# Performance work log

Hardware: AMD Instinct MI355X
Metric: run time of the kernel (lower is better)

Reference implementation:

```python
import jax, jax.numpy as jnp
import numpy as np

N_USER = 50000
N_ITEM = 50000
E = 800000
C_IN = 128
C_OUT = 128
N_HEADS = 4


def setup_inputs() -> dict:
    key = jax.random.key(0)
    ks = jax.random.split(key, 12)
    xav = lambda k, shp: jax.random.uniform(k, shp, jnp.float32, -1.0, 1.0) * jnp.sqrt(6.0 / (shp[0] + shp[1]))
    return {
        'x_user': jax.random.normal(ks[0], (N_USER, C_IN), jnp.float32),
        'x_item': jax.random.normal(ks[1], (N_ITEM, C_IN), jnp.float32),
        'ei_u2i': jnp.stack([jax.random.randint(ks[2], (E,), 0, N_USER, jnp.int32),
                             jax.random.randint(ks[3], (E,), 0, N_ITEM, jnp.int32)]),
        'ei_i2u': jnp.stack([jax.random.randint(ks[4], (E,), 0, N_ITEM, jnp.int32),
                             jax.random.randint(ks[5], (E,), 0, N_USER, jnp.int32)]),
        'W_nb': xav(ks[6], (C_OUT, C_IN)),
        'b_nb': jnp.zeros((C_OUT,), jnp.float32),
        'W_self': xav(ks[7], (C_OUT, C_IN)),
        'b_self': jnp.zeros((C_OUT,), jnp.float32),
        'in_proj_w': xav(ks[8], (3 * C_OUT, C_OUT)),
        'in_proj_b': jnp.zeros((3 * C_OUT,), jnp.float32),
        'out_proj_w': xav(ks[9], (C_OUT, C_OUT)),
        'out_proj_b': jnp.zeros((C_OUT,), jnp.float32),
    }


def _multi_aggr(h_src, edge_index, n_dst):
    """h_src: already lin_neighbor-transformed src features [N_src, C].
    Returns [n_dst, 4, C] stacked as [max, min, sum, mean] (torch_scatter semantics:
    empty segments -> 0; mean divides by clamp(count, 1))."""
    src, dst = edge_index[0], edge_index[1]
    msgs = h_src[src]  # [E, C]  (linear commutes with gather)
    s = jax.ops.segment_sum(msgs, dst, num_segments=n_dst)
    cnt = jax.ops.segment_sum(jnp.ones((msgs.shape[0],), msgs.dtype), dst, num_segments=n_dst)
    has = (cnt > 0)[:, None]
    mean = s / jnp.maximum(cnt, 1.0)[:, None]
    mx = jnp.where(has, jax.ops.segment_max(msgs, dst, num_segments=n_dst), 0.0)
    mn = jnp.where(has, jax.ops.segment_min(msgs, dst, num_segments=n_dst), 0.0)
    return jnp.stack([mx, mn, s, mean], axis=1)  # [n_dst, 4, C]


def _mha(tokens, in_proj_w, in_proj_b, out_proj_w, out_proj_b):
    """torch nn.MultiheadAttention (eval mode, batch_first=False). tokens: [S, N, C]."""
    S, N, C = tokens.shape
    H, Dh = N_HEADS, C // N_HEADS
    qkv = tokens @ in_proj_w.T + in_proj_b            # [S, N, 3C]
    q, k, v = jnp.split(qkv, 3, axis=-1)
    q = q.reshape(S, N, H, Dh) * (1.0 / jnp.sqrt(jnp.asarray(Dh, tokens.dtype)))
    k = k.reshape(S, N, H, Dh)
    v = v.reshape(S, N, H, Dh)
    scores = jnp.einsum('snhd,tnhd->nhst', q, k)       # [N, H, S, S]
    attn = jax.nn.softmax(scores, axis=-1)
    o = jnp.einsum('nhst,tnhd->snhd', attn, v).reshape(S, N, C)
    return o @ out_proj_w.T + out_proj_b               # [S, N, C]


def reference(x_user, x_item, ei_u2i, ei_i2u, W_nb, b_nb, W_self, b_self,
              in_proj_w, in_proj_b, out_proj_w, out_proj_b):
    # shared neighbor linear applied once per node type, then gathered per edge
    h_user = x_user @ W_nb.T + b_nb
    h_item = x_item @ W_nb.T + b_nb
    aggr_item = _multi_aggr(h_user, ei_u2i, N_ITEM)    # user->item : [N_item, 4, C]
    aggr_user = _multi_aggr(h_item, ei_i2u, N_USER)    # item->user : [N_user, 4, C]

    def per_type(x, aggr):
        self_feat = x @ W_self.T + b_self              # [N, C]
        # tokens: [self, max, min, sum, mean] -> [5, N, C]
        tokens = jnp.concatenate([self_feat[None], jnp.transpose(aggr, (1, 0, 2))], axis=0)
        attn_out = _mha(tokens, in_proj_w, in_proj_b, out_proj_w, out_proj_b)
        return self_feat + attn_out.mean(axis=0)

    out_user = per_type(x_user, aggr_user)
    out_item = per_type(x_item, aggr_item)
    return (out_user, out_item)
```

## Files before the change

### kernel.cpp

```cpp
#include <hip/hip_runtime.h>
#include <hip/hip_bf16.h>


#define C 128
#define NHEAD 4
#define DH 32
#define QK_SCALE 0.17677669529663687f

typedef __attribute__((ext_vector_type(8))) short bf16x8;
typedef __attribute__((ext_vector_type(4))) short short4v;
typedef __attribute__((ext_vector_type(2))) short short2v;
typedef __attribute__((ext_vector_type(4))) float f32x4;

__device__ __forceinline__ short f2bf(float f) {
    unsigned u = __float_as_uint(f);
    unsigned r = u + 0x7FFFu + ((u >> 16) & 1u);
    return (short)(r >> 16);
}

__global__ __launch_bounds__(256, 2) void transform_prep_kernel(
    const float* __restrict__ xu, const float* __restrict__ xi,
    int NU, int NTOT,
    const float* __restrict__ Wnb, const float* __restrict__ bnb,
    const float* __restrict__ Wself, const float* __restrict__ bself,
    float* __restrict__ h, float* __restrict__ selfout,
    const float* __restrict__ Wip, unsigned* __restrict__ img,
    int* __restrict__ curA, int nA, int* __restrict__ curB, int nB, int TB)
{
    const int tid = threadIdx.x;

    if ((int)blockIdx.x >= TB) {
        int bid2 = (int)blockIdx.x - TB;
        if (bid2 < 96) {
            int id = bid2 * 256 + tid;
            int ks = id / (384 * 16);
            int rem = id - ks * (384 * 16);
            int n = rem >> 4, kk = rem & 15;
            float a = Wip[(size_t)n * C + ks * 32 + kk * 2 + 0];
            float b = Wip[(size_t)n * C + ks * 32 + kk * 2 + 1];
            unsigned pa = ((unsigned)(unsigned short)f2bf(a))
                        | (((unsigned)(unsigned short)f2bf(b)) << 16);
            img[(size_t)ks * 6144 + n * 16 + kk] = pa;
        } else {
            int i = (bid2 - 96) * 256 + tid;
            if (i < nA) curA[i] = 0;
            else if (i < nA + nB) curB[i - nA] = 0;
        }
        return;
    }

    __shared__ float As[64 * 132];
    __shared__ float Bs[256 * 36];
    __shared__ float biasS[256];

    const int row0 = blockIdx.x * 64;

    biasS[tid] = (tid < 128) ? bnb[tid] : bself[tid - 128];

#pragma unroll
    for (int i = 0; i < 8; i++) {
        int id = tid + i * 256;
        int r = id >> 5, c4 = id & 31;
        int row = row0 + r;
        float4 v = make_float4(0.f, 0.f, 0.f, 0.f);
        if (row < NTOT) {
            v = (row < NU) ? ((const float4*)xu)[(size_t)row * 32 + c4]
                           : ((const float4*)xi)[(size_t)(row - NU) * 32 + c4];
        }
        *(float4*)&As[r * 132 + c4 * 4] = v;
    }

    const int tm = tid >> 5;
    const int tn = tid & 31;

    float acc[8][8];
#pragma unroll
    for (int m = 0; m < 8; m++)
#pragma unroll
        for (int j = 0; j < 8; j++) acc[m][j] = 0.f;

    for (int ks = 0; ks < 4; ks++) {
        __syncthreads();
#pragma unroll
        for (int i = 0; i < 8; i++) {
            int id = tid + i * 256;
            int n = id >> 3, q = id & 7;
            const float4* src = (n < 128)
                ? &((const float4*)Wnb)[(size_t)n * 32 + ks * 8 + q]
                : &((const float4*)Wself)[(size_t)(n - 128) * 32 + ks * 8 + q];
            *(float4*)&Bs[n * 36 + q * 4] = *src;
        }
        __syncthreads();

        for (int k4 = 0; k4 < 8; k4++) {
            float4 a[8];
#pragma unroll
            for (int m = 0; m < 8; m++)
                a[m] = *(const float4*)&As[(tm * 8 + m) * 132 + ks * 32 + k4 * 4];
            float4 b[8];
#pragma unroll
            for (int j = 0; j < 8; j++)
                b[j] = *(const float4*)&Bs[(tn + 32 * j) * 36 + k4 * 4];
#pragma unroll
            for (int m = 0; m < 8; m++) {
                float4 av = a[m];
#pragma unroll
                for (int j = 0; j < 8; j++) {
                    float4 bv = b[j];
                    acc[m][j] += av.x * bv.x + av.y * bv.y
                               + av.z * bv.z + av.w * bv.w;
                }
            }
        }
    }

#pragma unroll
    for (int m = 0; m < 8; m++) {
        int row = row0 + tm * 8 + m;
        if (row < NTOT) {
#pragma unroll
            for (int j = 0; j < 8; j++) {
                int jj = tn + 32 * j;
                float v = acc[m][j] + biasS[jj];
                if (j < 4) h[(size_t)row * C + jj] = v;
                else       selfout[(size_t)row * C + (jj - 128)] = v;
            }
        }
    }
}

__global__ __launch_bounds__(256) void hist2_kernel(
    const int* __restrict__ dstA, int nA, int* __restrict__ curA,
    const int* __restrict__ dstB, int nB, int* __restrict__ curB)
{
    int i = blockIdx.x * 256 + threadIdx.x;
    if (i < nA) atomicAdd(&curA[dstA[i]], 1);
    else if (i < nA + nB) atomicAdd(&curB[dstB[i - nA]], 1);
}

__global__ __launch_bounds__(1024) void scan2_kernel(
    int* __restrict__ curA, int nA, int* __restrict__ curB, int nB)
{
    int* cur = (blockIdx.x == 0) ? curA : curB;
    const int n = (blockIdx.x == 0) ? nA : nB;

    __shared__ int wsum[16];
    __shared__ int carryS;
    const int tid = threadIdx.x, lane = tid & 63, wv = tid >> 6;
    if (tid == 0) carryS = 0;
    __syncthreads();
    for (int base = 0; base < n; base += 4096) {
        int i0 = base + tid * 4;
        int v0 = 0, v1 = 0, v2 = 0, v3 = 0;
        if (i0 + 3 < n) {
            int4 t = *(const int4*)&cur[i0];
            v0 = t.x; v1 = t.y; v2 = t.z; v3 = t.w;
        } else {
            if (i0 < n) v0 = cur[i0];
            if (i0 + 1 < n) v1 = cur[i0 + 1];
            if (i0 + 2 < n) v2 = cur[i0 + 2];
            if (i0 + 3 < n) v3 = cur[i0 + 3];
        }
        int s1 = v0 + v1, s2 = s1 + v2, s3 = s2 + v3;
        int x = s3;
#pragma unroll
        for (int d = 1; d < 64; d <<= 1) {
            int t = __shfl_up(x, d, 64);
            if (lane >= d) x += t;
        }
        if (lane == 63) wsum[wv] = x;
        int carry = carryS;
        __syncthreads();
        int wpre = 0;
#pragma unroll
        for (int w2 = 0; w2 < 16; w2++) wpre += (w2 < wv) ? wsum[w2] : 0;
        int excl = x - s3 + wpre + carry;
        if (i0 + 3 < n) {
            int4 st; st.x = excl; st.y = excl + v0; st.z = excl + s1; st.w = excl + s2;
            *(int4*)&cur[i0] = st;
        } else {
            if (i0 < n) cur[i0] = excl;
            if (i0 + 1 < n) cur[i0 + 1] = excl + v0;
            if (i0 + 2 < n) cur[i0 + 2] = excl + s1;
            if (i0 + 3 < n) cur[i0 + 3] = excl + s2;
        }
        __syncthreads();
        if (tid == 0) {
            int t = 0;
#pragma unroll
            for (int w2 = 0; w2 < 16; w2++) t += wsum[w2];
            carryS = carry + t;
        }
        __syncthreads();
    }
}

__global__ __launch_bounds__(256) void fill2_kernel(
    const int* __restrict__ srcA, const int* __restrict__ dstA, int nA,
    int* __restrict__ curA, unsigned short* __restrict__ csrA,
    const int* __restrict__ srcB, const int* __restrict__ dstB, int nB,
    int* __restrict__ curB, unsigned short* __restrict__ csrB)
{
    int i = blockIdx.x * 256 + threadIdx.x;
    if (i < nA) {
        int p = atomicAdd(&curA[dstA[i]], 1);
        csrA[p] = (unsigned short)srcA[i];
    } else if (i < nA + nB) {
        int j = i - nA;
        int p = atomicAdd(&curB[dstB[j]], 1);
        csrB[p] = (unsigned short)srcB[j];
    }
}

#define ATN 4

__global__ __launch_bounds__(256, 8) void attn_fused_kernel(
    const float* __restrict__ h_src, const unsigned short* __restrict__ csr,
    const int* __restrict__ cur, const float* __restrict__ selfF,
    const short* __restrict__ wipbf, const float* __restrict__ bip,
    float* __restrict__ omean_g, int n_nodes)
{
    __shared__ char Ash[16 * 272];
    __shared__ float cinv[ATN];

    const int tid = threadIdx.x;
    const int lane = tid & 63;
    const int wv = tid >> 6;
    const int node0 = blockIdx.x * ATN;

    if (tid < 128) {
        int r = tid >> 5, c4 = tid & 31;
        int node = node0 + r;
        float4 v = make_float4(0.f, 0.f, 0.f, 0.f);
        if (node < n_nodes) v = ((const float4*)selfF)[(size_t)node * 32 + c4];
        short4v b;
        b.x = f2bf(v.x); b.y = f2bf(v.y); b.z = f2bf(v.z); b.w = f2bf(v.w);
        *(short4v*)(Ash + (r * 4) * 272 + c4 * 8) = b;
    }

    {
        const float2* h2 = (const float2*)h_src;
        int node = node0 + wv;
        float2 vs = make_float2(0.f, 0.f);
        float2 vmx = make_float2(-3.4e38f, -3.4e38f);
        float2 vmn = make_float2(3.4e38f, 3.4e38f);
        int deg = 0;
        if (node < n_nodes) {
            int start = (node == 0) ? 0 : cur[node - 1];
            int end = cur[node];
            deg = end - start;
            int e = start;
            for (; e + 8 <= end; e += 8) {
                float2 v[8];
#pragma unroll
                for (int i = 0; i < 8; i++) {
                    int s = csr[e + i];
                    v[i] = h2[(size_t)s * 64 + lane];
                }
#pragma unroll
                for (int i = 0; i < 8; i++) {
                    vs.x += v[i].x; vs.y += v[i].y;
                    vmx.x = fmaxf(vmx.x, v[i].x); vmx.y = fmaxf(vmx.y, v[i].y);
                    vmn.x = fminf(vmn.x, v[i].x); vmn.y = fminf(vmn.y, v[i].y);
                }
            }
            if (e < end) {
                int last = end - 1;
                float2 v[8];
#pragma unroll
                for (int i = 0; i < 8; i++) {
                    int idx = e + i;
                    int s = csr[(idx <= last) ? idx : last];
                    v[i] = h2[(size_t)s * 64 + lane];
                }
#pragma unroll
                for (int i = 0; i < 8; i++) {
                    if (e + i <= last) {
                        vs.x += v[i].x; vs.y += v[i].y;
                        vmx.x = fmaxf(vmx.x, v[i].x); vmx.y = fmaxf(vmx.y, v[i].y);
                        vmn.x = fminf(vmn.x, v[i].x); vmn.y = fminf(vmn.y, v[i].y);
                    }
                }
            }
        }
        if (deg == 0) {
            vmx = make_float2(0.f, 0.f);
            vmn = make_float2(0.f, 0.f);
        }
        short2v p;
        p.x = f2bf(vmx.x); p.y = f2bf(vmx.y);
        *(short2v*)(Ash + (wv * 4 + 1) * 272 + lane * 4) = p;
        p.x = f2bf(vmn.x); p.y = f2bf(vmn.y);
        *(short2v*)(Ash + (wv * 4 + 2) * 272 + lane * 4) = p;
        p.x = f2bf(vs.x); p.y = f2bf(vs.y);
        *(short2v*)(Ash + (wv * 4 + 3) * 272 + lane * 4) = p;
        if (lane == 0) cinv[wv] = 1.f / (float)max(deg, 1);
    }
    __syncthreads();

    const int quad = lane >> 4;
    const int col16 = lane & 15;

    f32x4 acc[6];
#pragma unroll
    for (int t = 0; t < 6; t++) acc[t] = (f32x4){0.f, 0.f, 0.f, 0.f};

#pragma unroll
    for (int ks = 0; ks < 4; ks++) {
        bf16x8 af = *(const bf16x8*)(Ash + col16 * 272 + ks * 64 + quad * 16);
#pragma unroll
        for (int t = 0; t < 6; t++) {
            int nb = wv * 32 + (t & 1) * 16 + (t >> 1) * 128 + col16;
            bf16x8 bfr = *(const bf16x8*)((const char*)wipbf
                          + (size_t)ks * 24576 + (size_t)nb * 64 + quad * 16);
            acc[t] = __builtin_amdgcn_mfma_f32_16x16x32_bf16(af, bfr, acc[t], 0, 0, 0);
        }
    }

    const float ci = cinv[quad];
    const float cis = ci * QK_SCALE;

    const float bq0 = bip[wv * 32 + col16];
    const float bq1 = bip[wv * 32 + 16 + col16];
    const float bk0 = bip[128 + wv * 32 + col16];
    const float bk1 = bip[128 + wv * 32 + 16 + col16];
    const float bv0 = bip[256 + wv * 32 + col16];
    const float bv1 = bip[256 + wv * 32 + 16 + col16];
    const float bq0s = bq0 * QK_SCALE;
    const float bq1s = bq1 * QK_SCALE;

    float k0[5], k1[5];
#pragma unroll
    for (int s = 0; s < 4; s++) { k0[s] = acc[2][s] + bk0; k1[s] = acc[3][s] + bk1; }
    k0[4] = fmaf(acc[2][3], ci, bk0);
    k1[4] = fmaf(acc[3][3], ci, bk1);

    float wj[5] = {0.f, 0.f, 0.f, 0.f, 0.f};
#pragma unroll
    for (int i = 0; i < 5; i++) {
        float qi0 = (i < 4) ? fmaf(acc[0][i], QK_SCALE, bq0s)
                            : fmaf(acc[0][3], cis, bq0s);
        float qi1 = (i < 4) ? fmaf(acc[1][i], QK_SCALE, bq1s)
                            : fmaf(acc[1][3], cis, bq1s);
        float sv[5];
#pragma unroll
        for (int j = 0; j < 5; j++) sv[j] = qi0 * k0[j] + qi1 * k1[j];
#pragma unroll
        for (int j = 0; j < 5; j++) {
            sv[j] += __shfl_xor(sv[j], 1, 16);
            sv[j] += __shfl_xor(sv[j], 2, 16);
            sv[j] += __shfl_xor(sv[j], 4, 16);
            sv[j] += __shfl_xor(sv[j], 8, 16);
        }
        float m = sv[0];
#pragma unroll
        for (int j = 1; j < 5; j++) m = fmaxf(m, sv[j]);
        float e[5], l = 0.f;
#pragma unroll
        for (int j = 0; j < 5; j++) { e[j] = __expf(sv[j] - m); l += e[j]; }
        float inv = 0.2f / l;
#pragma unroll
        for (int j = 0; j < 5; j++) wj[j] = fmaf(e[j], inv, wj[j]);
    }

    float o0 = 0.f, o1 = 0.f;
#pragma unroll
    for (int j = 0; j < 5; j++) {
        float v0 = (j < 4) ? (acc[4][j] + bv0) : fmaf(acc[4][3], ci, bv0);
        float v1 = (j < 4) ? (acc[5][j] + bv1) : fmaf(acc[5][3], ci, bv1);
        o0 = fmaf(wj[j], v0, o0);
        o1 = fmaf(wj[j], v1, o1);
    }

    int node = node0 + quad;
    if (node < n_nodes) {
        omean_g[(size_t)node * C + wv * 32 + col16] = o0;
        omean_g[(size_t)node * C + wv * 32 + 16 + col16] = o1;
    }
}

__global__ __launch_bounds__(256, 3) void outproj_kernel(
    const float* __restrict__ omean_g, const float* __restrict__ Wop,
    const float* __restrict__ bop, float* __restrict__ out, int M)
{
    __shared__ float As[64 * 132];
    __shared__ float Bs[128 * 36];
    __shared__ float bopS[C];

    const int tid = threadIdx.x;
    const int m0 = blockIdx.x * 64;

    if (tid < C) bopS[tid] = bop[tid];

#pragma unroll
    for (int i = 0; i < 8; i++) {
        int id = tid + i * 256;
        int r = id >> 5, c4 = id & 31;
        float4 v = make_float4(0.f, 0.f, 0.f, 0.f);
        if (m0 + r < M) v = ((const float4*)omean_g)[(size_t)(m0 + r) * 32 + c4];
        *(float4*)&As[r * 132 + c4 * 4] = v;
    }

    const int tn = tid & 31;
    const int tm = tid >> 5;
    float acc[8][4];
#pragma unroll
    for (int m = 0; m < 8; m++)
#pragma unroll
        for (int j = 0; j < 4; j++) acc[m][j] = 0.f;

    for (int ks = 0; ks < 4; ks++) {
        __syncthreads();
#pragma unroll
        for (int i = 0; i < 4; i++) {
            int id = tid + i * 256;
            int n = id >> 3, q = id & 7;
            float4 w = ((const float4*)Wop)[(size_t)n * 32 + ks * 8 + q];
            *(float4*)&Bs[n * 36 + q * 4] = w;
        }
        __syncthreads();

        for (int k4 = 0; k4 < 8; k4++) {
            float4 a[8];
#pragma unroll
            for (int m = 0; m < 8; m++)
                a[m] = *(const float4*)&As[(tm * 8 + m) * 132 + ks * 32 + k4 * 4];
            float4 b[4];
#pragma unroll
            for (int j = 0; j < 4; j++)
                b[j] = *(const float4*)&Bs[(tn + 32 * j) * 36 + k4 * 4];
#pragma unroll
            for (int m = 0; m < 8; m++) {
                float4 av = a[m];
#pragma unroll
                for (int j = 0; j < 4; j++) {
                    float4 bv = b[j];
                    acc[m][j] += av.x * bv.x + av.y * bv.y
                               + av.z * bv.z + av.w * bv.w;
                }
            }
        }
    }

#pragma unroll
    for (int m = 0; m < 8; m++) {
        int row = m0 + tm * 8 + m;
        if (row < M) {
#pragma unroll
            for (int j = 0; j < 4; j++) {
                int col = tn + 32 * j;
                float* o = &out[(size_t)row * C + col];
                *o += acc[m][j] + bopS[col];
            }
        }
    }
}

extern "C" void kernel_launch(void* const* d_in, const int* in_sizes, int n_in,
                              void* d_out, int out_size, void* d_ws, size_t ws_size,
                              hipStream_t stream) {
    const float* x_user = (const float*)d_in[0];
    const float* x_item = (const float*)d_in[1];
    const int*   ei_u2i = (const int*)d_in[2];
    const int*   ei_i2u = (const int*)d_in[3];
    const float* W_nb   = (const float*)d_in[4];
    const float* b_nb   = (const float*)d_in[5];
    const float* W_self = (const float*)d_in[6];
    const float* b_self = (const float*)d_in[7];
    const float* Wip    = (const float*)d_in[8];
    const float* bip    = (const float*)d_in[9];
    const float* Wop    = (const float*)d_in[10];
    const float* bop    = (const float*)d_in[11];

    const int NU = in_sizes[0] / C;
    const int NI = in_sizes[1] / C;
    const int E1 = in_sizes[2] / 2;
    const int E2 = in_sizes[3] / 2;
    const int NTOT = NU + NI;

    float* out_user = (float*)d_out;
    float* out_item = out_user + (size_t)NU * C;

    float* ws = (float*)d_ws;
    short* wipbf     = (short*)ws;
    float* h_all     = ws + 24576;
    const size_t rc = (size_t)NTOT * C;
    float* omean_all = h_all + rc;
    int*   curA      = (int*)(omean_all + rc);
    int*   curB      = curA + NI;
    unsigned short* csrA16 = (unsigned short*)(curB + NU);
    unsigned short* csrB16 = csrA16 + E1;

    float* h_user = h_all;
    float* h_item = h_all + (size_t)NU * C;
    float* om_user = omean_all;
    float* om_item = omean_all + (size_t)NU * C;

    const int TB = (NTOT + 63) / 64;
    const int PB = 96 + (NTOT + 255) / 256;
    transform_prep_kernel<<<TB + PB, 256, 0, stream>>>(
        x_user, x_item, NU, NTOT, W_nb, b_nb, W_self, b_self,
        h_all, (float*)d_out, Wip, (unsigned*)wipbf, curA, NI, curB, NU, TB);

    hist2_kernel<<<(E1 + E2 + 255) / 256, 256, 0, stream>>>(
        ei_u2i + E1, E1, curA, ei_i2u + E2, E2, curB);

    scan2_kernel<<<2, 1024, 0, stream>>>(curA, NI, curB, NU);

    fill2_kernel<<<(E1 + E2 + 255) / 256, 256, 0, stream>>>(
        ei_u2i, ei_u2i + E1, E1, curA, csrA16,
        ei_i2u, ei_i2u + E2, E2, curB, csrB16);

    attn_fused_kernel<<<(NU + ATN - 1) / ATN, 256, 0, stream>>>(
        h_item, csrB16, curB, out_user, wipbf, bip, om_user, NU);

    attn_fused_kernel<<<(NI + ATN - 1) / ATN, 256, 0, stream>>>(
        h_user, csrA16, curA, out_item, wipbf, bip, om_item, NI);

    outproj_kernel<<<(NTOT + 63) / 64, 256, 0, stream>>>(
        omean_all, Wop, bop, (float*)d_out, NTOT);
}
```

Measured before the change: 706.8 us.

## Fuse histogram, scan and CSR fill into one cooperative grid-synced kernel

Replaces the separate histogram, two-block scan and fill kernels with one cooperative kernel of 2048 blocks that uses grid.sync between phases. The scan becomes a parallel block-level scan with per-block partials, replacing a serial 2-block scan. The aim is to cut launch overhead and the serialized single-block scan latency. If the cooperative launch fails it falls back to the old three kernels. The kernel hardcodes 1024 blocks per graph, so it assumes node counts of at most 262144 per type. Grid-wide syncs add barrier cost.

```diff
diff --git a/kernel.cpp b/kernel.cpp
--- a/kernel.cpp
+++ b/kernel.cpp
@@ -1,5 +1,8 @@
 #include <hip/hip_runtime.h>
 #include <hip/hip_bf16.h>
+#include <hip/hip_cooperative_groups.h>
+
+namespace cg = cooperative_groups;
 
 
 #define C 128
@@ -129,6 +132,90 @@
     }
 }
 
+__global__ __launch_bounds__(256, 8) void graph_build_kernel(
+    const int* __restrict__ dstA, const int* __restrict__ srcA, int nEA,
+    int* __restrict__ curA, unsigned short* __restrict__ csrA, int nA,
+    const int* __restrict__ dstB, const int* __restrict__ srcB, int nEB,
+    int* __restrict__ curB, unsigned short* __restrict__ csrB, int nB,
+    int* __restrict__ partials)
+{
+    cg::grid_group grid = cg::this_grid();
+    const int tid = threadIdx.x;
+    const int bid = (int)blockIdx.x;
+    const int gsz = (int)gridDim.x * 256;
+    const int gid = bid * 256 + tid;
+
+    for (int i = gid; i < nEA + nEB; i += gsz) {
+        if (i < nEA) atomicAdd(&curA[dstA[i]], 1);
+        else         atomicAdd(&curB[dstB[i - nEA]], 1);
+    }
+    grid.sync();
+
+    const bool isB = (bid >= 1024);
+    int* cur = isB ? curB : curA;
+    const int n = isB ? nB : nA;
+    int* part = partials + (isB ? 1024 : 0);
+    const int bl = isB ? bid - 1024 : bid;
+    const int idx = bl * 256 + tid;
+    const int lane = tid & 63, wv = tid >> 6;
+
+    int v = (idx < n) ? cur[idx] : 0;
+    int x = v;
+#pragma unroll
+    for (int d = 1; d < 64; d <<= 1) {
+        int t = __shfl_up(x, d, 64);
+        if (lane >= d) x += t;
+    }
+    __shared__ int wsum[4];
+    if (lane == 63) wsum[wv] = x;
+    __syncthreads();
+    int wpre = 0;
+#pragma unroll
+    for (int w = 0; w < 4; w++) wpre += (w < wv) ? wsum[w] : 0;
+    const int excl = x - v + wpre;
+    if (tid == 0) part[bl] = wsum[0] + wsum[1] + wsum[2] + wsum[3];
+    grid.sync();
+
+    if (bid < 2) {
+        int* p = partials + bid * 1024;
+        int pv0 = p[tid * 4 + 0], pv1 = p[tid * 4 + 1];
+        int pv2 = p[tid * 4 + 2], pv3 = p[tid * 4 + 3];
+        int s0 = pv0, s1 = s0 + pv1, s2 = s1 + pv2, s3 = s2 + pv3;
+        int xx = s3;
+#pragma unroll
+        for (int d = 1; d < 64; d <<= 1) {
+            int t = __shfl_up(xx, d, 64);
+            if (lane >= d) xx += t;
+        }
+        __shared__ int wsum2[4];
+        if (lane == 63) wsum2[wv] = xx;
+        __syncthreads();
+        int wpre2 = 0;
+#pragma unroll
+        for (int w = 0; w < 4; w++) wpre2 += (w < wv) ? wsum2[w] : 0;
+        int base = xx - s3 + wpre2;
+        p[tid * 4 + 0] = base;
+        p[tid * 4 + 1] = base + s0;
+        p[tid * 4 + 2] = base + s1;
+        p[tid * 4 + 3] = base + s2;
+    }
+    grid.sync();
+
+    if (idx < n) cur[idx] = excl + part[bl];
+    grid.sync();
+
+    for (int i = gid; i < nEA + nEB; i += gsz) {
+        if (i < nEA) {
+            int p2 = atomicAdd(&curA[dstA[i]], 1);
+            csrA[p2] = (unsigned short)srcA[i];
+        } else {
+            int j = i - nEA;
+            int p2 = atomicAdd(&curB[dstB[j]], 1);
+            csrB[p2] = (unsigned short)srcB[j];
+        }
+    }
+}
+
 __global__ __launch_bounds__(256) void hist2_kernel(
     const int* __restrict__ dstA, int nA, int* __restrict__ curA,
     const int* __restrict__ dstB, int nB, int* __restrict__ curB)
@@ -490,6 +577,7 @@
     int*   curB      = curA + NI;
     unsigned short* csrA16 = (unsigned short*)(curB + NU);
     unsigned short* csrB16 = csrA16 + E1;
+    int*   partials  = (int*)(csrB16 + E2);
 
     float* h_user = h_all;
     float* h_item = h_all + (size_t)NU * C;
@@ -502,14 +590,25 @@
         x_user, x_item, NU, NTOT, W_nb, b_nb, W_self, b_self,
         h_all, (float*)d_out, Wip, (unsigned*)wipbf, curA, NI, curB, NU, TB);
 
-    hist2_kernel<<<(E1 + E2 + 255) / 256, 256, 0, stream>>>(
-        ei_u2i + E1, E1, curA, ei_i2u + E2, E2, curB);
-
-    scan2_kernel<<<2, 1024, 0, stream>>>(curA, NI, curB, NU);
-
-    fill2_kernel<<<(E1 + E2 + 255) / 256, 256, 0, stream>>>(
-        ei_u2i, ei_u2i + E1, E1, curA, csrA16,
-        ei_i2u, ei_i2u + E2, E2, curB, csrB16);
+    {
+        const int* dA = ei_u2i + E1; const int* sA = ei_u2i; int eA = E1; int na = NI;
+        const int* dB = ei_i2u + E2; const int* sB = ei_i2u; int eB = E2; int nb = NU;
+        void* args[] = { (void*)&dA, (void*)&sA, (void*)&eA,
+                         (void*)&curA, (void*)&csrA16, (void*)&na,
+                         (void*)&dB, (void*)&sB, (void*)&eB,
+                         (void*)&curB, (void*)&csrB16, (void*)&nb,
+                         (void*)&partials };
+        hipError_t cerr = hipLaunchCooperativeKernel(
+            (const void*)graph_build_kernel, dim3(2048), dim3(256), args, 0, stream);
+        if (cerr != hipSuccess) {
+            hist2_kernel<<<(E1 + E2 + 255) / 256, 256, 0, stream>>>(
+                ei_u2i + E1, E1, curA, ei_i2u + E2, E2, curB);
+            scan2_kernel<<<2, 1024, 0, stream>>>(curA, NI, curB, NU);
+            fill2_kernel<<<(E1 + E2 + 255) / 256, 256, 0, stream>>>(
+                ei_u2i, ei_u2i + E1, E1, curA, csrA16,
+                ei_i2u, ei_i2u + E2, E2, curB, csrB16);
+        }
+    }
 
     attn_fused_kernel<<<(NU + ATN - 1) / ATN, 256, 0, stream>>>(
         h_item, csrB16, curB, out_user, wipbf, bip, om_user, NU);
```

Result: slower. 1.500 ms (+112.1%).
